# Kernel tuning notes

Measured on AMD Instinct MI355X. Metric: run time of the kernel, lower is better.

Reference implementation:

```python
import jax, jax.numpy as jnp
import numpy as np

DIM = 1024
N_HEADS = 16
HEAD_DIM = DIM // N_HEADS
HIDDEN = 4096  # round_up(4*DIM, 256)
ROPE_THETA = 10000.0
EPS = 1e-6


def setup_inputs() -> dict:
    key = jax.random.key(0)
    ks = jax.random.split(key, 10)
    s = 0.02
    return {
        "x": jax.random.normal(ks[0], (1, 4096, DIM), dtype=jnp.float32),
        "wq": jax.random.normal(ks[1], (DIM, DIM), dtype=jnp.float32) * s,
        "wk": jax.random.normal(ks[2], (DIM, DIM), dtype=jnp.float32) * s,
        "wv": jax.random.normal(ks[3], (DIM, DIM), dtype=jnp.float32) * s,
        "wo": jax.random.normal(ks[4], (DIM, DIM), dtype=jnp.float32) * s,
        "w1": jax.random.normal(ks[5], (HIDDEN, DIM), dtype=jnp.float32) * s,
        "w2": jax.random.normal(ks[6], (DIM, HIDDEN), dtype=jnp.float32) * s,
        "w3": jax.random.normal(ks[7], (HIDDEN, DIM), dtype=jnp.float32) * s,
        "g_attn": jnp.ones((DIM,), dtype=jnp.float32),
        "g_ffn": jnp.ones((DIM,), dtype=jnp.float32),
    }


def _rmsnorm(x, g):
    return x * jax.lax.rsqrt(jnp.mean(x * x, axis=-1, keepdims=True) + EPS) * g


def _rope_tables(seqlen):
    inv = 1.0 / (ROPE_THETA ** (jnp.arange(0, HEAD_DIM, 2, dtype=jnp.float32) / HEAD_DIM))
    ang = jnp.arange(seqlen, dtype=jnp.float32)[:, None] * inv[None, :]  # [s, hd/2]
    return jnp.cos(ang), jnp.sin(ang)


def _apply_rope(q, cos, sin):
    # q: [b, s, h, hd]; pairs (even, odd) treated as complex (re, im)
    b, s, h, d = q.shape
    qr = q.reshape(b, s, h, d // 2, 2)
    re, im = qr[..., 0], qr[..., 1]
    c = cos[None, :, None, :]
    sn = sin[None, :, None, :]
    out = jnp.stack([re * c - im * sn, re * sn + im * c], axis=-1)
    return out.reshape(b, s, h, d)


def reference(x, wq, wk, wv, wo, w1, w2, w3, g_attn, g_ffn):
    b, s, _ = x.shape
    xn = _rmsnorm(x, g_attn)
    q = (xn @ wq.T).reshape(b, s, N_HEADS, HEAD_DIM)
    k = (xn @ wk.T).reshape(b, s, N_HEADS, HEAD_DIM)
    v = (xn @ wv.T).reshape(b, s, N_HEADS, HEAD_DIM)
    cos, sin = _rope_tables(s)
    q = _apply_rope(q, cos, sin)
    k = _apply_rope(k, cos, sin)
    scores = jnp.einsum("bthd,bThd->bhtT", q, k) / np.sqrt(HEAD_DIM).astype(np.float32)
    probs = jax.nn.softmax(scores, axis=-1)
    attn = jnp.einsum("bhtT,bThd->bthd", probs, v).reshape(b, s, DIM)
    h = x + attn @ wo.T
    hn = _rmsnorm(h, g_ffn)
    ff = (jax.nn.silu(hn @ w1.T) * (hn @ w3.T)) @ w2.T
    return h + ff
```

## Files before the change

kernel.cpp:

```cpp
#include <hip/hip_runtime.h>

#define S_LEN 4096
#define DIMM  1024
#define NH    16
#define HD    64
#define HID   4096

typedef unsigned short u16;
typedef __attribute__((ext_vector_type(8))) short bf16x8;
typedef __attribute__((ext_vector_type(4))) short short4b;
typedef __attribute__((ext_vector_type(8))) unsigned short u16x8;
typedef __attribute__((ext_vector_type(4))) float f32x4;

__device__ __forceinline__ u16 f2bf(float f) {
  unsigned u = __float_as_uint(f);
  u += 0x7fffu + ((u >> 16) & 1u);
  return (u16)(u >> 16);
}
__device__ __forceinline__ float bf2f(u16 h) {
  return __uint_as_float(((unsigned)h) << 16);
}
__device__ __forceinline__ unsigned pack_bf16(float hi, float lo) {
  return __builtin_amdgcn_perm(__float_as_uint(hi), __float_as_uint(lo), 0x07060302u);
}
__device__ __forceinline__ float fexp2(float x) { return __builtin_amdgcn_exp2f(x); }

__device__ __forceinline__ void gl_lds16(const void* g, void* l) {
  __builtin_amdgcn_global_load_lds(
      (const __attribute__((address_space(1))) void*)g,
      (__attribute__((address_space(3))) void*)l, 16, 0, 0);
}

__device__ __forceinline__ f32x4 mfma16(short4b a, short4b b, f32x4 c) {
#if __has_builtin(__builtin_amdgcn_mfma_f32_16x16x16bf16_1k)
  return __builtin_amdgcn_mfma_f32_16x16x16bf16_1k(a, b, c, 0, 0, 0);
#else
  asm("v_mfma_f32_16x16x16_bf16 %0, %1, %2, %0" : "+v"(c) : "v"(a), "v"(b));
  return c;
#endif
}

__global__ __launch_bounds__(256) void prep_kernel(
    const float* __restrict__ wq, const float* __restrict__ wk, const float* __restrict__ wv,
    const float* __restrict__ wo, const float* __restrict__ w1, const float* __restrict__ w3,
    const float* __restrict__ w2, const float* __restrict__ x, const float* __restrict__ g_attn,
    u16* __restrict__ wqkb, u16* __restrict__ wvb, u16* __restrict__ wob,
    u16* __restrict__ w13b, u16* __restrict__ w2b, u16* __restrict__ xnb,
    float* __restrict__ cosT, float* __restrict__ sinT) {
  int b = blockIdx.x;
  int t = threadIdx.x;
  if (b < 8192) {
    const float* src;
    u16* dst;
    int i;
    if (b < 2048) {
      int which = b >> 9, lb = b & 511;
      src = which == 0 ? wq : which == 1 ? wk : which == 2 ? wv : wo;
      dst = which == 0 ? wqkb : which == 1 ? (wqkb + (1 << 20)) : which == 2 ? wvb : wob;
      i = (lb * 256 + t) * 8;
    } else {
      int b2 = b - 2048, which = b2 >> 11, lb = b2 & 2047;
      src = which == 0 ? w1 : which == 1 ? w3 : w2;
      dst = which == 0 ? w13b : which == 1 ? (w13b + (4 << 20)) : w2b;
      i = (lb * 256 + t) * 8;
    }
    float4 a = *(const float4*)(src + i);
    float4 c = *(const float4*)(src + i + 4);
    u16x8 r;
    r[0] = f2bf(a.x); r[1] = f2bf(a.y); r[2] = f2bf(a.z); r[3] = f2bf(a.w);
    r[4] = f2bf(c.x); r[5] = f2bf(c.y); r[6] = f2bf(c.z); r[7] = f2bf(c.w);
    *(u16x8*)(dst + i) = r;
  } else if (b < 8704) {
    int idx = (b - 8192) * 256 + t;
    int pos = idx >> 5, i = idx & 31;
    double inv = pow(10000.0, -(double)(2 * i) / 64.0);
    double a = (double)pos * inv;
    cosT[idx] = (float)cos(a);
    sinT[idx] = (float)sin(a);
  } else {
    int row = b - 8704;
    const float4 v = *(const float4*)(x + (size_t)row * DIMM + t * 4);
    float ss = v.x * v.x + v.y * v.y + v.z * v.z + v.w * v.w;
#pragma unroll
    for (int off = 32; off > 0; off >>= 1) ss += __shfl_down(ss, off);
    __shared__ float red[4];
    if ((t & 63) == 0) red[t >> 6] = ss;
    __syncthreads();
    float tot = red[0] + red[1] + red[2] + red[3];
    float sc = rsqrtf(tot * (1.0f / DIMM) + 1e-6f);
    const float4 gv = *(const float4*)(g_attn + t * 4);
    ushort4 o;
    o.x = f2bf(v.x * sc * gv.x);
    o.y = f2bf(v.y * sc * gv.y);
    o.z = f2bf(v.z * sc * gv.z);
    o.w = f2bf(v.w * sc * gv.w);
    *(ushort4*)(xnb + (size_t)row * DIMM + t * 4) = o;
  }
}

__global__ __launch_bounds__(256) void rmsnorm_kernel(const float* __restrict__ x, const float* __restrict__ g,
                                                      u16* __restrict__ out) {
  int row = blockIdx.x;
  int t = threadIdx.x;
  const float4 v = *(const float4*)(x + (size_t)row * DIMM + t * 4);
  float ss = v.x * v.x + v.y * v.y + v.z * v.z + v.w * v.w;
#pragma unroll
  for (int off = 32; off > 0; off >>= 1) ss += __shfl_down(ss, off);
  __shared__ float red[4];
  if ((t & 63) == 0) red[t >> 6] = ss;
  __syncthreads();
  float tot = red[0] + red[1] + red[2] + red[3];
  float sc = rsqrtf(tot * (1.0f / DIMM) + 1e-6f);
  const float4 gv = *(const float4*)(g + t * 4);
  ushort4 o;
  o.x = f2bf(v.x * sc * gv.x);
  o.y = f2bf(v.y * sc * gv.y);
  o.z = f2bf(v.z * sc * gv.z);
  o.w = f2bf(v.w * sc * gv.w);
  *(ushort4*)(out + (size_t)row * DIMM + t * 4) = o;
}

template <int OUTMODE>
__global__ __launch_bounds__(512) void gemm_kernel(const u16* __restrict__ A, const u16* __restrict__ B,
                                                   void* Cout, const float* res, int N, int K, int lda,
                                                   const float* cosT, const float* sinT) {
  __shared__ uint4 As0[1024], Bs0[1024], As1[1024], Bs1[1024];
  const int t = threadIdx.x;
  const int w = t >> 6, l = t & 63;
  const int wm = w >> 1, wn = w & 1;
  const int bm = blockIdx.y, bn = blockIdx.x;
  const int quad = l >> 4, lc = l & 15;

  f32x4 acc[2][4];
  const f32x4 zero = {0.0f, 0.0f, 0.0f, 0.0f};
#pragma unroll
  for (int mi = 0; mi < 2; mi++)
#pragma unroll
    for (int ni = 0; ni < 4; ni++) acc[mi][ni] = zero;

  const int band0 = t >> 6, kq0 = (t >> 4) & 3, row0 = t & 15;
  const u16* Ap0 = A + (size_t)(bm * 128 + band0 * 16 + row0) * lda + kq0 * 8;
  const u16* Bp0 = B + (size_t)(bn * 128 + band0 * 16 + row0) * K + kq0 * 8;
  const int abase = wm * 128 + l;
  const int bbase = wn * 256 + l;

#define STAGEL(AD, BD, K0)                 \
  do {                                     \
    gl_lds16(Ap0 + (K0), &(AD)[t]);        \
    gl_lds16(Ap0 + (K0) + 32, &(AD)[t + 512]); \
    gl_lds16(Bp0 + (K0), &(BD)[t]);        \
    gl_lds16(Bp0 + (K0) + 32, &(BD)[t + 512]); \
  } while (0)

#define COMPL(AS, BS)                                                                               \
  do {                                                                                              \
    _Pragma("unroll") for (int ks = 0; ks < 2; ks++) {                                              \
      bf16x8 af[2], bfr[4];                                                                         \
      _Pragma("unroll") for (int mi = 0; mi < 2; mi++)                                              \
          af[mi] = *(const bf16x8*)&(AS)[ks * 512 + abase + mi * 64];                               \
      _Pragma("unroll") for (int ni = 0; ni < 4; ni++)                                              \
          bfr[ni] = *(const bf16x8*)&(BS)[ks * 512 + bbase + ni * 64];                              \
      _Pragma("unroll") for (int mi = 0; mi < 2; mi++)                                              \
          _Pragma("unroll") for (int ni = 0; ni < 4; ni++)                                          \
              acc[mi][ni] = __builtin_amdgcn_mfma_f32_16x16x32_bf16(af[mi], bfr[ni], acc[mi][ni], 0, 0, 0); \
    }                                                                                               \
  } while (0)

  STAGEL(As0, Bs0, 0);
  __syncthreads();
  int k0 = 0;
  for (; k0 + 128 < K; k0 += 128) {
    STAGEL(As1, Bs1, k0 + 64);
    COMPL(As0, Bs0);
    __syncthreads();
    STAGEL(As0, Bs0, k0 + 128);
    COMPL(As1, Bs1);
    __syncthreads();
  }
  STAGEL(As1, Bs1, k0 + 64);
  COMPL(As0, Bs0);
  __syncthreads();
  COMPL(As1, Bs1);
#undef STAGEL
#undef COMPL

  const int rbase = bm * 128 + wm * 32 + quad * 4;
  const int cbase = bn * 128 + wn * 64 + lc;
#pragma unroll
  for (int mi = 0; mi < 2; mi++) {
#pragma unroll
    for (int r = 0; r < 4; r++) {
      int row = rbase + mi * 16 + r;
#pragma unroll
      for (int ni = 0; ni < 4; ni++) {
        int col = cbase + ni * 16;
        if constexpr (OUTMODE == 0) {
          ((u16*)Cout)[(size_t)row * N + col] = f2bf(acc[mi][ni][r]);
        } else if constexpr (OUTMODE == 1) {
          size_t idx = (size_t)row * N + col;
          ((float*)Cout)[idx] = res[idx] + acc[mi][ni][r];
        } else if constexpr (OUTMODE == 2) {
          int h = row >> 6, din = row & 63;
          int kb = col >> 6, k63 = col & 63;
          int off = ((h << 6) + kb) * 4096 + (((din >> 4) << 1) + (k63 >> 5)) * 512 +
                    ((((k63 >> 2) & 3) << 4) + (din & 15)) * 8 + ((k63 >> 4) & 1) * 4 + (k63 & 3);
          ((u16*)Cout)[off] = f2bf(acc[mi][ni][r]);
        } else {
          float v = acc[mi][ni][r];
          float pv = __shfl_xor(v, 1);
          int i = ((ni * 16 + lc) & 63) >> 1;
          float c = cosT[(row << 5) + i], s = sinT[(row << 5) + i];
          float o = (lc & 1) ? (pv * s + v * c) : (v * c - pv * s);
          ((u16*)Cout)[(size_t)row * N + col] = f2bf(o);
        }
      }
    }
  }
}

__global__ __launch_bounds__(512) void gemm256_kernel(const u16* __restrict__ A, const u16* __restrict__ B,
                                                      u16* __restrict__ Cout, int N, int K, int lda) {
  __shared__ uint4 As0[1024], Bs0[1024], As1[1024], Bs1[1024];
  const int t = threadIdx.x;
  const int w = t >> 6, l = t & 63;
  const int wm = w >> 2, wn = w & 3;
  const int bm = blockIdx.y, bn = blockIdx.x;
  const int quad = l >> 4, lc = l & 15;

  f32x4 acc[8][4];
  const f32x4 zero = {0.0f, 0.0f, 0.0f, 0.0f};
#pragma unroll
  for (int mi = 0; mi < 8; mi++)
#pragma unroll
    for (int ni = 0; ni < 4; ni++) acc[mi][ni] = zero;

  const int band0 = t >> 6, kq0 = (t >> 4) & 3, row0 = t & 15;
  const u16* Ap0 = A + (size_t)(bm * 256 + band0 * 16 + row0) * lda + kq0 * 8;
  const u16* Bp0 = B + (size_t)(bn * 256 + band0 * 16 + row0) * K + kq0 * 8;
  const size_t Astep = (size_t)128 * lda;
  const size_t Bstep = (size_t)128 * K;

#define STAGE256(AD, BD, K0)                      \
  do {                                            \
    gl_lds16(Ap0 + (K0), &(AD)[t]);               \
    gl_lds16(Ap0 + Astep + (K0), &(AD)[t + 512]); \
    gl_lds16(Bp0 + (K0), &(BD)[t]);               \
    gl_lds16(Bp0 + Bstep + (K0), &(BD)[t + 512]); \
  } while (0)

#define COMPUTE256(AS, BS)                                                                          \
  do {                                                                                              \
    bf16x8 af[8], bfr[4];                                                                           \
    _Pragma("unroll") for (int mi = 0; mi < 8; mi++)                                                \
        af[mi] = *(const bf16x8*)&(AS)[(wm * 8 + mi) * 64 + l];                                     \
    _Pragma("unroll") for (int ni = 0; ni < 4; ni++)                                                \
        bfr[ni] = *(const bf16x8*)&(BS)[(wn * 4 + ni) * 64 + l];                                    \
    _Pragma("unroll") for (int mi = 0; mi < 8; mi++)                                                \
        _Pragma("unroll") for (int ni = 0; ni < 4; ni++)                                            \
            acc[mi][ni] = __builtin_amdgcn_mfma_f32_16x16x32_bf16(af[mi], bfr[ni], acc[mi][ni], 0, 0, 0); \
  } while (0)

  STAGE256(As0, Bs0, 0);
  __syncthreads();

  int k0 = 0;
  for (; k0 + 64 < K; k0 += 64) {
    STAGE256(As1, Bs1, k0 + 32);
    COMPUTE256(As0, Bs0);
    __syncthreads();
    STAGE256(As0, Bs0, k0 + 64);
    COMPUTE256(As1, Bs1);
    __syncthreads();
  }
  STAGE256(As1, Bs1, k0 + 32);
  COMPUTE256(As0, Bs0);
  __syncthreads();
  COMPUTE256(As1, Bs1);
#undef STAGE256
#undef COMPUTE256

  const int rbase = bm * 256 + wm * 128 + quad * 4;
  const int cbase = bn * 256 + wn * 64 + lc;
#pragma unroll
  for (int mi = 0; mi < 8; mi++) {
#pragma unroll
    for (int r = 0; r < 4; r++) {
      int row = rbase + mi * 16 + r;
#pragma unroll
      for (int ni = 0; ni < 4; ni++) {
        int col = cbase + ni * 16;
        Cout[(size_t)row * N + col] = f2bf(acc[mi][ni][r]);
      }
    }
  }
}

__global__ __launch_bounds__(512) void attn_kernel(const u16* __restrict__ Qm, const u16* __restrict__ Km,
                                                   const u16* __restrict__ Vsw, u16* __restrict__ Om) {
  __shared__ char smem[32768];
  uint4* Ks0 = (uint4*)smem;
  uint4* Vs0 = (uint4*)(smem + 8192);
  uint4* Ks1 = (uint4*)(smem + 16384);
  uint4* Vs1 = (uint4*)(smem + 24576);
  const int t = threadIdx.x;
  const int w = t >> 6, l = t & 63;
  const int quad = l >> 4, lc = l & 15;
  const int hd = blockIdx.y;
  const int qrow = blockIdx.x * 128 + w * 16;

  bf16x8 qf_[2];
#pragma unroll
  for (int ch = 0; ch < 2; ch++)
    qf_[ch] = *(const bf16x8*)(Qm + (size_t)(qrow + lc) * 2048 + hd * HD + ch * 32 + quad * 8);

  const f32x4 zero = {0.0f, 0.0f, 0.0f, 0.0f};
  f32x4 Oa[4];
#pragma unroll
  for (int df = 0; df < 4; df++) Oa[df] = zero;
  float mt = -1e30f, ls = 0.0f;

  const int s0 = t >> 7, c0 = (t >> 6) & 1, kq0 = (t >> 4) & 3, row0 = t & 15;
  const u16* Kp0 = Km + (size_t)(s0 * 16 + row0) * 2048 + hd * HD + c0 * 32 + kq0 * 8;
  const u16* Vp = Vsw + (size_t)(hd * HD) * 4096 + t * 8;
  const float csc = 0.125f * 1.44269504088896f;

#define STAGEKV(KD, VD, TT)                                  \
  do {                                                       \
    gl_lds16(Kp0 + (size_t)(TT)*131072, &(KD)[t]);           \
    gl_lds16(Vp + (size_t)(TT)*4096, &(VD)[t]);              \
  } while (0)

#define TILE_COMPUTE(KS, VS)                                                                 \
  do {                                                                                       \
    f32x4 Sf[4];                                                                             \
    _Pragma("unroll") for (int kf = 0; kf < 4; kf++) {                                       \
      bf16x8 ka = *(const bf16x8*)&(KS)[kf * 128 + l];                                       \
      bf16x8 kb2 = *(const bf16x8*)&(KS)[kf * 128 + 64 + l];                                 \
      f32x4 z = __builtin_amdgcn_mfma_f32_16x16x32_bf16(ka, qf_[0], zero, 0, 0, 0);          \
      z = __builtin_amdgcn_mfma_f32_16x16x32_bf16(kb2, qf_[1], z, 0, 0, 0);                  \
      Sf[kf] = z * csc;                                                                      \
    }                                                                                        \
    float tmax = -1e30f;                                                                     \
    _Pragma("unroll") for (int kf = 0; kf < 4; kf++)                                         \
        _Pragma("unroll") for (int r = 0; r < 4; r++) tmax = fmaxf(tmax, Sf[kf][r]);         \
    tmax = fmaxf(tmax, __shfl_xor(tmax, 16));                                                \
    tmax = fmaxf(tmax, __shfl_xor(tmax, 32));                                                \
    if (!__all(tmax <= mt + 8.0f)) {                                                        \
      float mnew = fmaxf(mt, tmax);                                                          \
      float alpha = fexp2(mt - mnew);                                                        \
      mt = mnew;                                                                             \
      ls *= alpha;                                                                           \
      _Pragma("unroll") for (int df = 0; df < 4; df++) Oa[df] *= alpha;                      \
    }                                                                                        \
    float psum = 0.0f;                                                                       \
    _Pragma("unroll") for (int kf = 0; kf < 4; kf++)                                         \
        _Pragma("unroll") for (int r = 0; r < 4; r++) {                                      \
      float p = fexp2(Sf[kf][r] - mt);                                                       \
      Sf[kf][r] = p;                                                                         \
      psum += p;                                                                             \
    }                                                                                        \
    psum += __shfl_xor(psum, 16);                                                            \
    psum += __shfl_xor(psum, 32);                                                            \
    ls += psum;                                                                              \
    short4b pk[4];                                                                           \
    _Pragma("unroll") for (int kf = 0; kf < 4; kf++) {                                       \
      union { short4b s4; uint2 u2; } cv;                                                    \
      cv.u2.x = pack_bf16(Sf[kf][1], Sf[kf][0]);                                             \
      cv.u2.y = pack_bf16(Sf[kf][3], Sf[kf][2]);                                             \
      pk[kf] = cv.s4;                                                                        \
    }                                                                                        \
    _Pragma("unroll") for (int df = 0; df < 4; df++)                                         \
        _Pragma("unroll") for (int tp = 0; tp < 2; tp++) {                                   \
      union { bf16x8 v8; short4b h[2]; } vv;                                                 \
      vv.v8 = *(const bf16x8*)&(VS)[(df * 2 + tp) * 64 + l];                                 \
      Oa[df] = mfma16(vv.h[0], pk[2 * tp], Oa[df]);                                          \
      Oa[df] = mfma16(vv.h[1], pk[2 * tp + 1], Oa[df]);                                      \
    }                                                                                        \
  } while (0)

  STAGEKV(Ks0, Vs0, 0);
  __syncthreads();

  for (int tt = 0; tt < 64; tt += 2) {
    STAGEKV(Ks1, Vs1, tt + 1);
    TILE_COMPUTE(Ks0, Vs0);
    __syncthreads();
    if (tt + 2 < 64) STAGEKV(Ks0, Vs0, tt + 2);
    TILE_COMPUTE(Ks1, Vs1);
    __syncthreads();
  }
#undef STAGEKV
#undef TILE_COMPUTE

  u16* ep = (u16*)smem;
  float invl = 1.0f / ls;
#pragma unroll
  for (int df = 0; df < 4; df++) {
    int qb = w * 16 + lc;
    int d = df * 16 + quad * 4;
    uint2 pv;
    pv.x = pack_bf16(Oa[df][1] * invl, Oa[df][0] * invl);
    pv.y = pack_bf16(Oa[df][3] * invl, Oa[df][2] * invl);
    *(uint2*)(ep + qb * 72 + d) = pv;
  }
  __syncthreads();
#pragma unroll
  for (int it = 0; it < 2; it++) {
    int qb = it * 64 + (t >> 3);
    int dp = (t & 7) * 8;
    u16x8 rowv = *(const u16x8*)(ep + qb * 72 + dp);
    *(u16x8*)(Om + (size_t)(blockIdx.x * 128 + qb) * DIMM + hd * HD + dp) = rowv;
  }
}

__global__ __launch_bounds__(256) void silu_mul_kernel(u16* __restrict__ u13) {
  int i = (blockIdx.x * 256 + threadIdx.x) * 8;
  int r = i >> 12, c = i & 4095;
  u16* up = u13 + (size_t)r * 8192 + c;
  u16x8 uv = *(const u16x8*)up;
  u16x8 gv = *(const u16x8*)(up + 4096);
  u16x8 o;
#pragma unroll
  for (int j = 0; j < 8; j++) {
    float a = bf2f(uv[j]);
    float b = bf2f(gv[j]);
    float sv = a / (1.0f + __expf(-a));
    o[j] = f2bf(sv * b);
  }
  *(u16x8*)up = o;
}

extern "C" void kernel_launch(void* const* d_in, const int* in_sizes, int n_in,
                              void* d_out, int out_size, void* d_ws, size_t ws_size,
                              hipStream_t stream) {
  const float* x      = (const float*)d_in[0];
  const float* wq     = (const float*)d_in[1];
  const float* wk     = (const float*)d_in[2];
  const float* wv     = (const float*)d_in[3];
  const float* wo     = (const float*)d_in[4];
  const float* w1     = (const float*)d_in[5];
  const float* w2     = (const float*)d_in[6];
  const float* w3     = (const float*)d_in[7];
  const float* g_attn = (const float*)d_in[8];
  const float* g_ffn  = (const float*)d_in[9];
  float* out = (float*)d_out;
  char* ws = (char*)d_ws;
  const size_t MB = 1ull << 20;

  u16* wqkb = (u16*)(ws + 0 * MB);
  u16* wvb  = (u16*)(ws + 4 * MB);
  u16* wob  = (u16*)(ws + 6 * MB);
  u16* w13b = (u16*)(ws + 8 * MB);
  u16* w2b  = (u16*)(ws + 24 * MB);
  u16* xnb  = (u16*)(ws + 32 * MB);
  u16* qkb  = (u16*)(ws + 40 * MB);
  u16* vswz = (u16*)(ws + 56 * MB);
  u16* attb = (u16*)(ws + 64 * MB);
  u16* u13  = (u16*)(ws + 40 * MB);
  float* cosT = (float*)(ws + 104 * MB);
  float* sinT = (float*)(ws + 104 * MB + 512 * 1024);

  prep_kernel<<<12800, 256, 0, stream>>>(wq, wk, wv, wo, w1, w3, w2, x, g_attn,
                                         wqkb, wvb, wob, w13b, w2b, xnb, cosT, sinT);

  gemm_kernel<3><<<dim3(16, 32), 512, 0, stream>>>(xnb, wqkb, qkb, nullptr, 2048, DIMM, DIMM, cosT, sinT);
  gemm_kernel<2><<<dim3(32, 8), 512, 0, stream>>>(wvb, xnb, vswz, nullptr, S_LEN, DIMM, DIMM, nullptr, nullptr);

  attn_kernel<<<dim3(32, 16), 512, 0, stream>>>(qkb, qkb + 1024, vswz, attb);

  gemm_kernel<1><<<dim3(8, 32), 512, 0, stream>>>(attb, wob, out, x, DIMM, DIMM, DIMM, nullptr, nullptr);

  rmsnorm_kernel<<<4096, 256, 0, stream>>>(out, g_ffn, xnb);

  gemm256_kernel<<<dim3(32, 16), 512, 0, stream>>>(xnb, w13b, u13, 8192, DIMM, DIMM);

  silu_mul_kernel<<<8192, 256, 0, stream>>>(u13);

  gemm_kernel<1><<<dim3(8, 32), 512, 0, stream>>>(u13, w2b, out, out, DIMM, HID, 8192, nullptr, nullptr);
}
```

Before: 536.0 us.

## Process two query groups per wave in attention and fold softmax scale into Q

The attention kernel drops from 8 to 4 waves per block, and each wave now handles 32 query rows as two 16-row groups. Each K and V fragment read from LDS is therefore reused for twice as many MFMAs, halving LDS traffic per unit of compute. Each thread now stages twice as many K/V loads. Separately, the softmax scale (1/sqrt(d)·log2e) is applied to Q in the QK GEMM epilogue, which removes the per-tile multiply in attention. The trade-off is higher register pressure and fewer waves to hide latency.

Result: no change. 544.7 us (+1.6%).

```diff
diff --git a/kernel.cpp b/kernel.cpp
--- a/kernel.cpp
+++ b/kernel.cpp
@@ -186,6 +186,7 @@
 
   const int rbase = bm * 128 + wm * 32 + quad * 4;
   const int cbase = bn * 128 + wn * 64 + lc;
+  const float qs = (OUTMODE == 3 && bn < 8) ? 0.18033688011112f : 1.0f;
 #pragma unroll
   for (int mi = 0; mi < 2; mi++) {
 #pragma unroll
@@ -211,7 +212,7 @@
           int i = ((ni * 16 + lc) & 63) >> 1;
           float c = cosT[(row << 5) + i], s = sinT[(row << 5) + i];
           float o = (lc & 1) ? (pv * s + v * c) : (v * c - pv * s);
-          ((u16*)Cout)[(size_t)row * N + col] = f2bf(o);
+          ((u16*)Cout)[(size_t)row * N + col] = f2bf(o * qs);
         }
       }
     }
@@ -295,7 +296,7 @@
   }
 }
 
-__global__ __launch_bounds__(512) void attn_kernel(const u16* __restrict__ Qm, const u16* __restrict__ Km,
+__global__ __launch_bounds__(256) void attn_kernel(const u16* __restrict__ Qm, const u16* __restrict__ Km,
                                                    const u16* __restrict__ Vsw, u16* __restrict__ Om) {
   __shared__ char smem[32768];
   uint4* Ks0 = (uint4*)smem;
@@ -306,75 +307,87 @@
   const int w = t >> 6, l = t & 63;
   const int quad = l >> 4, lc = l & 15;
   const int hd = blockIdx.y;
-  const int qrow = blockIdx.x * 128 + w * 16;
-
-  bf16x8 qf_[2];
-#pragma unroll
-  for (int ch = 0; ch < 2; ch++)
-    qf_[ch] = *(const bf16x8*)(Qm + (size_t)(qrow + lc) * 2048 + hd * HD + ch * 32 + quad * 8);
+  const int qrow = blockIdx.x * 128 + w * 32;
+
+  bf16x8 qf_[2][2];
+#pragma unroll
+  for (int g = 0; g < 2; g++)
+#pragma unroll
+    for (int ch = 0; ch < 2; ch++)
+      qf_[g][ch] = *(const bf16x8*)(Qm + (size_t)(qrow + g * 16 + lc) * 2048 + hd * HD + ch * 32 + quad * 8);
 
   const f32x4 zero = {0.0f, 0.0f, 0.0f, 0.0f};
-  f32x4 Oa[4];
-#pragma unroll
-  for (int df = 0; df < 4; df++) Oa[df] = zero;
-  float mt = -1e30f, ls = 0.0f;
-
-  const int s0 = t >> 7, c0 = (t >> 6) & 1, kq0 = (t >> 4) & 3, row0 = t & 15;
-  const u16* Kp0 = Km + (size_t)(s0 * 16 + row0) * 2048 + hd * HD + c0 * 32 + kq0 * 8;
+  f32x4 Oa[2][4];
+#pragma unroll
+  for (int g = 0; g < 2; g++)
+#pragma unroll
+    for (int df = 0; df < 4; df++) Oa[g][df] = zero;
+  float mt[2] = {-1e30f, -1e30f}, ls[2] = {0.0f, 0.0f};
+
+  const int t2 = t + 256;
+  const u16* KpA = Km + (size_t)((t >> 7) * 16 + (t & 15)) * 2048 + hd * HD + ((t >> 6) & 1) * 32 + ((t >> 4) & 3) * 8;
+  const u16* KpB = Km + (size_t)((t2 >> 7) * 16 + (t2 & 15)) * 2048 + hd * HD + ((t2 >> 6) & 1) * 32 + ((t2 >> 4) & 3) * 8;
   const u16* Vp = Vsw + (size_t)(hd * HD) * 4096 + t * 8;
-  const float csc = 0.125f * 1.44269504088896f;
-
-#define STAGEKV(KD, VD, TT)                                  \
-  do {                                                       \
-    gl_lds16(Kp0 + (size_t)(TT)*131072, &(KD)[t]);           \
-    gl_lds16(Vp + (size_t)(TT)*4096, &(VD)[t]);              \
+
+#define STAGEKV(KD, VD, TT)                                   \
+  do {                                                        \
+    gl_lds16(KpA + (size_t)(TT)*131072, &(KD)[t]);            \
+    gl_lds16(KpB + (size_t)(TT)*131072, &(KD)[t + 256]);      \
+    gl_lds16(Vp + (size_t)(TT)*4096, &(VD)[t]);               \
+    gl_lds16(Vp + 2048 + (size_t)(TT)*4096, &(VD)[t + 256]);  \
   } while (0)
 
 #define TILE_COMPUTE(KS, VS)                                                                 \
   do {                                                                                       \
-    f32x4 Sf[4];                                                                             \
+    f32x4 Sf[2][4];                                                                          \
     _Pragma("unroll") for (int kf = 0; kf < 4; kf++) {                                       \
       bf16x8 ka = *(const bf16x8*)&(KS)[kf * 128 + l];                                       \
       bf16x8 kb2 = *(const bf16x8*)&(KS)[kf * 128 + 64 + l];                                 \
-      f32x4 z = __builtin_amdgcn_mfma_f32_16x16x32_bf16(ka, qf_[0], zero, 0, 0, 0);          \
-      z = __builtin_amdgcn_mfma_f32_16x16x32_bf16(kb2, qf_[1], z, 0, 0, 0);                  \
-      Sf[kf] = z * csc;                                                                      \
+      _Pragma("unroll") for (int g = 0; g < 2; g++) {                                        \
+        f32x4 z = __builtin_amdgcn_mfma_f32_16x16x32_bf16(ka, qf_[g][0], zero, 0, 0, 0);     \
+        z = __builtin_amdgcn_mfma_f32_16x16x32_bf16(kb2, qf_[g][1], z, 0, 0, 0);             \
+        Sf[g][kf] = z;                                                                       \
+      }                                                                                      \
     }                                                                                        \
-    float tmax = -1e30f;                                                                     \
-    _Pragma("unroll") for (int kf = 0; kf < 4; kf++)                                         \
-        _Pragma("unroll") for (int r = 0; r < 4; r++) tmax = fmaxf(tmax, Sf[kf][r]);         \
-    tmax = fmaxf(tmax, __shfl_xor(tmax, 16));                                                \
-    tmax = fmaxf(tmax, __shfl_xor(tmax, 32));                                                \
-    if (!__all(tmax <= mt + 8.0f)) {                                                        \
-      float mnew = fmaxf(mt, tmax);                                                          \
-      float alpha = fexp2(mt - mnew);                                                        \
-      mt = mnew;                                                                             \
-      ls *= alpha;                                                                           \
-      _Pragma("unroll") for (int df = 0; df < 4; df++) Oa[df] *= alpha;                      \
-    }                                                                                        \
-    float psum = 0.0f;                                                                       \
-    _Pragma("unroll") for (int kf = 0; kf < 4; kf++)                                         \
-        _Pragma("unroll") for (int r = 0; r < 4; r++) {                                      \
-      float p = fexp2(Sf[kf][r] - mt);                                                       \
-      Sf[kf][r] = p;                                                                         \
-      psum += p;                                                                             \
-    }                                                                                        \
-    psum += __shfl_xor(psum, 16);                                                            \
-    psum += __shfl_xor(psum, 32);                                                            \
-    ls += psum;                                                                              \
-    short4b pk[4];                                                                           \
-    _Pragma("unroll") for (int kf = 0; kf < 4; kf++) {                                       \
-      union { short4b s4; uint2 u2; } cv;                                                    \
-      cv.u2.x = pack_bf16(Sf[kf][1], Sf[kf][0]);                                             \
-      cv.u2.y = pack_bf16(Sf[kf][3], Sf[kf][2]);                                             \
-      pk[kf] = cv.s4;                                                                        \
+    short4b pk[2][4];                                                                        \
+    _Pragma("unroll") for (int g = 0; g < 2; g++) {                                          \
+      float tmax = -1e30f;                                                                   \
+      _Pragma("unroll") for (int kf = 0; kf < 4; kf++)                                       \
+          _Pragma("unroll") for (int r = 0; r < 4; r++) tmax = fmaxf(tmax, Sf[g][kf][r]);    \
+      tmax = fmaxf(tmax, __shfl_xor(tmax, 16));                                              \
+      tmax = fmaxf(tmax, __shfl_xor(tmax, 32));                                              \
+      if (!__all(tmax <= mt[g] + 8.0f)) {                                                    \
+        float mnew = fmaxf(mt[g], tmax);                                                     \
+        float alpha = fexp2(mt[g] - mnew);                                                   \
+        mt[g] = mnew;                                                                        \
+        ls[g] *= alpha;                                                                      \
+        _Pragma("unroll") for (int df = 0; df < 4; df++) Oa[g][df] *= alpha;                 \
+      }                                                                                      \
+      float psum = 0.0f;                                                                     \
+      _Pragma("unroll") for (int kf = 0; kf < 4; kf++)                                       \
+          _Pragma("unroll") for (int r = 0; r < 4; r++) {                                    \
+        float p = fexp2(Sf[g][kf][r] - mt[g]);                                               \
+        Sf[g][kf][r] = p;                                                                    \
+        psum += p;                                                                           \
+      }                                                                                      \
+      psum += __shfl_xor(psum, 16);                                                          \
+      psum += __shfl_xor(psum, 32);                                                          \
+      ls[g] += psum;                                                                         \
+      _Pragma("unroll") for (int kf = 0; kf < 4; kf++) {                                     \
+        union { short4b s4; uint2 u2; } cv;                                                  \
+        cv.u2.x = pack_bf16(Sf[g][kf][1], Sf[g][kf][0]);                                     \
+        cv.u2.y = pack_bf16(Sf[g][kf][3], Sf[g][kf][2]);                                     \
+        pk[g][kf] = cv.s4;                                                                   \
+      }                                                                                      \
     }                                                                                        \
     _Pragma("unroll") for (int df = 0; df < 4; df++)                                         \
         _Pragma("unroll") for (int tp = 0; tp < 2; tp++) {                                   \
       union { bf16x8 v8; short4b h[2]; } vv;                                                 \
       vv.v8 = *(const bf16x8*)&(VS)[(df * 2 + tp) * 64 + l];                                 \
-      Oa[df] = mfma16(vv.h[0], pk[2 * tp], Oa[df]);                                          \
-      Oa[df] = mfma16(vv.h[1], pk[2 * tp + 1], Oa[df]);                                      \
+      _Pragma("unroll") for (int g = 0; g < 2; g++) {                                        \
+        Oa[g][df] = mfma16(vv.h[0], pk[g][2 * tp], Oa[g][df]);                               \
+        Oa[g][df] = mfma16(vv.h[1], pk[g][2 * tp + 1], Oa[g][df]);                           \
+      }                                                                                      \
     }                                                                                        \
   } while (0)
 
@@ -393,20 +406,23 @@
 #undef TILE_COMPUTE
 
   u16* ep = (u16*)smem;
-  float invl = 1.0f / ls;
-#pragma unroll
-  for (int df = 0; df < 4; df++) {
-    int qb = w * 16 + lc;
-    int d = df * 16 + quad * 4;
-    uint2 pv;
-    pv.x = pack_bf16(Oa[df][1] * invl, Oa[df][0] * invl);
-    pv.y = pack_bf16(Oa[df][3] * invl, Oa[df][2] * invl);
-    *(uint2*)(ep + qb * 72 + d) = pv;
-  }
-  __syncthreads();
-#pragma unroll
-  for (int it = 0; it < 2; it++) {
-    int qb = it * 64 + (t >> 3);
+#pragma unroll
+  for (int g = 0; g < 2; g++) {
+    float invl = 1.0f / ls[g];
+#pragma unroll
+    for (int df = 0; df < 4; df++) {
+      int qb = w * 32 + g * 16 + lc;
+      int d = df * 16 + quad * 4;
+      uint2 pv;
+      pv.x = pack_bf16(Oa[g][df][1] * invl, Oa[g][df][0] * invl);
+      pv.y = pack_bf16(Oa[g][df][3] * invl, Oa[g][df][2] * invl);
+      *(uint2*)(ep + qb * 72 + d) = pv;
+    }
+  }
+  __syncthreads();
+#pragma unroll
+  for (int it = 0; it < 4; it++) {
+    int qb = it * 32 + (t >> 3);
     int dp = (t & 7) * 8;
     u16x8 rowv = *(const u16x8*)(ep + qb * 72 + dp);
     *(u16x8*)(Om + (size_t)(blockIdx.x * 128 + qb) * DIMM + hd * HD + dp) = rowv;
@@ -466,7 +482,7 @@
   gemm_kernel<3><<<dim3(16, 32), 512, 0, stream>>>(xnb, wqkb, qkb, nullptr, 2048, DIMM, DIMM, cosT, sinT);
   gemm_kernel<2><<<dim3(32, 8), 512, 0, stream>>>(wvb, xnb, vswz, nullptr, S_LEN, DIMM, DIMM, nullptr, nullptr);
 
-  attn_kernel<<<dim3(32, 16), 512, 0, stream>>>(qkb, qkb + 1024, vswz, attb);
+  attn_kernel<<<dim3(32, 16), 256, 0, stream>>>(qkb, qkb + 1024, vswz, attb);
 
   gemm_kernel<1><<<dim3(8, 32), 512, 0, stream>>>(attb, wob, out, x, DIMM, DIMM, DIMM, nullptr, nullptr);
 
```
